# Kernel optimization log

Hardware: AMD Instinct MI355X
Metric: run time of the kernel (lower is better)

## Reference

```python
import jax, jax.numpy as jnp
import numpy as np

EPS = 1e-12
TEMPERATURE = 0.1
QUEUE_SIZE = 1024
CUTOFF_KM = 25.0
EARTH_R_KM = 6371.0088


def _normalize(x, axis=-1):
    n = jnp.linalg.norm(x, axis=axis, keepdims=True)
    return x / jnp.maximum(n, EPS)


def _haversine_km(a, b):
    # a: (B,1,2), b: (1,S,2) in degrees (lat, lon) -> (B,S) km
    ra, rb = jnp.deg2rad(a), jnp.deg2rad(b)
    dlat = rb[..., 0] - ra[..., 0]
    dlon = rb[..., 1] - ra[..., 1]
    h = jnp.sin(dlat / 2) ** 2 + jnp.cos(ra[..., 0]) * jnp.cos(rb[..., 0]) * jnp.sin(dlon / 2) ** 2
    return 2.0 * EARTH_R_KM * jnp.arcsin(jnp.sqrt(jnp.clip(h, 0.0, 1.0)))


def setup_inputs() -> dict:
    key = jax.random.key(0)
    k1, k2, k3, k4, k5 = jax.random.split(key, 5)
    A, B, F, S = 3, 256, 512, 100000
    V = jax.random.normal(k1, (A, B, F), dtype=jnp.float32)
    L = jax.random.normal(k2, (B, F), dtype=jnp.float32)
    # gps as (lat, lon) degrees
    gps = jax.random.uniform(k3, (B, 2), dtype=jnp.float32) * jnp.array([120.0, 360.0]) - jnp.array([60.0, 180.0])
    support_feats = jax.random.normal(k4, (S, F), dtype=jnp.float32)
    support_gps = jax.random.uniform(k5, (S, 2), dtype=jnp.float32) * jnp.array([120.0, 360.0]) - jnp.array([60.0, 180.0])
    return {"V": V, "L": L, "gps": gps, "support_feats": support_feats, "support_gps": support_gps}


def reference(V, L, gps, support_feats, support_gps):
    T, Q = TEMPERATURE, QUEUE_SIZE
    L_norm = _normalize(L, axis=1)                      # (B,F)
    org = _normalize(V[0] * L_norm, axis=1)             # (B,F)
    aug = _normalize(V[1:] * L_norm, axis=2)            # (A-1,B,F)

    # nearest_neighbours (no_grad): per-batch NN in support set by dot-product sim
    sims = jnp.einsum('sf,bf->sb', support_feats, org)  # (S,B)
    nn_idx = jnp.argmax(sims, axis=0)                   # (B,)
    nn = _normalize(support_feats[nn_idx], axis=1)      # (B,F)
    nn = jax.lax.stop_gradient(nn)

    pos = jnp.exp(jnp.einsum('abf,bf->ab', aug, nn) / T)  # (A-1,B)
    batch_den = jnp.sum(pos, axis=0)                       # (B,)

    # nn_negative_queue (no_grad): first Q support rows farther than 25 km, zeros if fewer
    dist = _haversine_km(gps[:, None, :], support_gps[None, :, :])  # (B,S)
    far = dist > CUTOFF_KM                                          # (B,S)
    order = jnp.argsort(jnp.logical_not(far), axis=1)[:, :Q]        # stable: far rows first, in order
    valid = jnp.take_along_axis(far, order, axis=1)                 # (B,Q)
    negq = jnp.where(valid[..., None], support_feats[order], 0.0)   # (B,Q,F)
    negq = jax.lax.stop_gradient(_normalize(negq, axis=2))          # zero rows stay zero

    queue_den = jnp.sum(jnp.exp(jnp.einsum('bqf,bf->bq', negq, nn) / T), axis=1)  # (B,)

    loss = jnp.mean(-batch_den / (batch_den + queue_den))
    return loss
```

## Files before the change

### kernel.cpp

```cpp
#include <hip/hip_runtime.h>
#include <hip/hip_bf16.h>
#include <math.h>

#define B_N 256
#define F_N 512
#define S_N 100000
#define Q_N 1024
#define EPSF 1e-12f
#define BM 128
#define NBLK ((S_N + BM - 1) / BM)
#define CAND_MAX 64
#define MARGIN 0.125f

typedef __attribute__((ext_vector_type(8))) short short8v;
typedef __attribute__((ext_vector_type(4))) float f32x4;

__device__ __forceinline__ unsigned short f2bf(float x) {
  unsigned u = __float_as_uint(x);
  u = u + 0x7FFFu + ((u >> 16) & 1u);
  return (unsigned short)(u >> 16);
}

__device__ __forceinline__ float warpReduceSum(float v) {
  #pragma unroll
  for (int o = 32; o > 0; o >>= 1) v += __shfl_down(v, o);
  return v;
}

__device__ __forceinline__ float blockReduceSum256(float v, float* buf) {
  v = warpReduceSum(v);
  int lane = threadIdx.x & 63, w = threadIdx.x >> 6;
  __syncthreads();
  if (lane == 0) buf[w] = v;
  __syncthreads();
  return buf[0] + buf[1] + buf[2] + buf[3];
}

__device__ __forceinline__ void async_copy16(void* lds, const void* g) {
  __builtin_amdgcn_global_load_lds(
      (const __attribute__((address_space(1))) unsigned int*)g,
      (__attribute__((address_space(3))) unsigned int*)lds, 16, 0, 0);
}

__device__ __forceinline__ void cvt8hi(const float4 a, const float4 b,
                                       short8v& hi) {
  union { unsigned u[4]; short8v v; } H;
  union { __hip_bfloat162 b2; unsigned u; } c;
  c.b2 = __float22bfloat162_rn(make_float2(a.x, a.y)); H.u[0] = c.u;
  c.b2 = __float22bfloat162_rn(make_float2(a.z, a.w)); H.u[1] = c.u;
  c.b2 = __float22bfloat162_rn(make_float2(b.x, b.y)); H.u[2] = c.u;
  c.b2 = __float22bfloat162_rn(make_float2(b.z, b.w)); H.u[3] = c.u;
  hi = H.v;
}

__global__ __launch_bounds__(256) void k_prep(const float* __restrict__ V,
    const float* __restrict__ L, unsigned short* __restrict__ orghi,
    float* __restrict__ org, float* __restrict__ aug) {
  __shared__ float buf[4];
  int b = blockIdx.x, t = threadIdx.x;
  const float2 lv = *(const float2*)&L[b * F_N + t * 2];
  float ss = blockReduceSum256(lv.x * lv.x + lv.y * lv.y, buf);
  float invL = 1.0f / fmaxf(sqrtf(ss), EPSF);
  float lnx = lv.x * invL, lny = lv.y * invL;
  #pragma unroll
  for (int a = 0; a < 3; ++a) {
    const float2 vv = *(const float2*)&V[(a * B_N + b) * F_N + t * 2];
    float yx = vv.x * lnx, yy = vv.y * lny;
    float s2 = blockReduceSum256(yx * yx + yy * yy, buf);
    float inv = 1.0f / fmaxf(sqrtf(s2), EPSF);
    if (a == 0) {
      float ox = yx * inv, oy = yy * inv;
      int f = t * 2;
      int kt = f >> 5, kk = f & 31, sub = kk >> 3, pos = kk & 7;
      int off = kt * 8192 + b * 32 + ((sub ^ ((b >> 1) & 3)) << 3) + pos;
      ushort2 hv; hv.x = f2bf(ox); hv.y = f2bf(oy);
      *(ushort2*)&orghi[off] = hv;
      float2 of; of.x = ox; of.y = oy;
      *(float2*)&org[b * F_N + f] = of;
    } else {
      float* dst = &aug[((a - 1) * B_N + b) * F_N + t * 2];
      dst[0] = yx * inv;
      dst[1] = yy * inv;
    }
  }
}

__global__ __launch_bounds__(256, 2) void k_sims(const float* __restrict__ support,
    const unsigned short* __restrict__ orghi, float* __restrict__ blkmax) {
  __shared__ __align__(16) unsigned char smem[32768];

  int t = threadIdx.x;
  int lane = t & 63, w = t >> 6;
  int r15 = lane & 15, ks = lane >> 4;
  int s0 = blockIdx.x * BM;

  f32x4 acc0[16], acc1[16];
  #pragma unroll
  for (int n = 0; n < 16; ++n) {
    acc0[n] = (f32x4){0.f, 0.f, 0.f, 0.f};
    acc1[n] = (f32x4){0.f, 0.f, 0.f, 0.f};
  }

  int row0 = s0 + w * 32 + r15;
  int row1 = row0 + 16;
  if (row0 > S_N - 1) row0 = S_N - 1;
  if (row1 > S_N - 1) row1 = S_N - 1;
  const float* ap0 = support + (size_t)row0 * F_N + ks * 8;
  const float* ap1 = support + (size_t)row1 * F_N + ks * 8;

  const unsigned char* bsrc = (const unsigned char*)orghi + t * 16;

  {
    unsigned char* dst = smem + t * 16;
    #pragma unroll
    for (int p = 0; p < 4; ++p) async_copy16(dst + p * 4096, bsrc + p * 4096);
  }
  __builtin_amdgcn_sched_barrier(0);
  float4 a0a = *(const float4*)(ap0);
  float4 a0b = *(const float4*)(ap0 + 4);
  float4 a1a = *(const float4*)(ap1);
  float4 a1b = *(const float4*)(ap1 + 4);
  __builtin_amdgcn_sched_barrier(0);
  __syncthreads();

  const int rbase = r15 * 64 + ((ks ^ ((r15 >> 1) & 3)) << 4);

  #pragma unroll 1
  for (int kt = 0; kt < 16; ++kt) {
    unsigned char* bbuf = smem + (kt & 1) * 16384;
    short8v fh0, fh1;
    cvt8hi(a0a, a0b, fh0);
    cvt8hi(a1a, a1b, fh1);
    if (kt < 15) {
      const unsigned char* src = bsrc + (kt + 1) * 16384;
      unsigned char* dst = smem + ((kt + 1) & 1) * 16384 + t * 16;
      #pragma unroll
      for (int p = 0; p < 4; ++p) async_copy16(dst + p * 4096, src + p * 4096);
      __builtin_amdgcn_sched_barrier(0);
      a0a = *(const float4*)(ap0 + (kt + 1) * 32);
      a0b = *(const float4*)(ap0 + (kt + 1) * 32 + 4);
      a1a = *(const float4*)(ap1 + (kt + 1) * 32);
      a1b = *(const float4*)(ap1 + (kt + 1) * 32 + 4);
      __builtin_amdgcn_sched_barrier(0);
    }
    const unsigned char* bp = bbuf + rbase;
    __builtin_amdgcn_s_setprio(1);
    #pragma unroll
    for (int n = 0; n < 16; ++n) {
      short8v bh = *(const short8v*)(bp + n * 1024);
      acc0[n] = __builtin_amdgcn_mfma_f32_16x16x32_bf16(fh0, bh, acc0[n], 0, 0, 0);
      acc1[n] = __builtin_amdgcn_mfma_f32_16x16x32_bf16(fh1, bh, acc1[n], 0, 0, 0);
    }
    __builtin_amdgcn_s_setprio(0);
    __builtin_amdgcn_sched_barrier(0);
    if (kt < 15) {
      asm volatile("s_waitcnt vmcnt(4)" ::: "memory");
      __builtin_amdgcn_s_barrier();
    } else {
      __syncthreads();
    }
    __builtin_amdgcn_sched_barrier(0);
  }

  float* wkf = (float*)smem;
  #pragma unroll
  for (int n = 0; n < 16; ++n) {
    float bv = -INFINITY;
    #pragma unroll
    for (int r = 0; r < 4; ++r) {
      bv = fmaxf(bv, acc0[n][r]);
      bv = fmaxf(bv, acc1[n][r]);
    }
    bv = fmaxf(bv, __shfl_xor(bv, 16));
    bv = fmaxf(bv, __shfl_xor(bv, 32));
    if (lane < 16) wkf[w * 256 + n * 16 + lane] = bv;
  }
  __syncthreads();
  {
    float m4 = fmaxf(fmaxf(wkf[t], wkf[256 + t]),
                     fmaxf(wkf[512 + t], wkf[768 + t]));
    blkmax[(size_t)t * NBLK + blockIdx.x] = m4;
  }
}

__global__ __launch_bounds__(256) void k_picknn(const float* __restrict__ support,
    const float* __restrict__ org, const float* __restrict__ blkmax,
    int* __restrict__ nnidx) {
  __shared__ float orgs[F_N];
  __shared__ float redf[4];
  __shared__ int lcand[CAND_MAX];
  __shared__ int lcnt;
  __shared__ double rv[4];
  __shared__ int ri[4];
  int b = blockIdx.x, t = threadIdx.x;
  int lane = t & 63, w = t >> 6;

  orgs[t] = org[b * F_N + t];
  orgs[256 + t] = org[b * F_N + 256 + t];
  if (t == 0) lcnt = 0;

  const float* bm = blkmax + (size_t)b * NBLK;
  float mx = -INFINITY;
  for (int rb = t; rb < NBLK; rb += 256) mx = fmaxf(mx, bm[rb]);
  #pragma unroll
  for (int o = 32; o > 0; o >>= 1) mx = fmaxf(mx, __shfl_xor(mx, o));
  __syncthreads();
  if (lane == 0) redf[w] = mx;
  __syncthreads();
  mx = fmaxf(fmaxf(redf[0], redf[1]), fmaxf(redf[2], redf[3]));
  float thr = mx - MARGIN;

  for (int rb = t; rb < NBLK; rb += 256) {
    if (bm[rb] >= thr) {
      int sl = atomicAdd(&lcnt, 1);
      if (sl < CAND_MAX) lcand[sl] = rb;
    }
  }
  __syncthreads();
  int nc = lcnt < CAND_MAX ? lcnt : CAND_MAX;

  double bv = -1e300;
  int bi = 0x7FFFFFFF;
  for (int task = t; task < nc * BM; task += 256) {
    int c = task >> 7, r = task & (BM - 1);
    int s = lcand[c] * BM + r;
    if (s < S_N) {
      const float* rp = support + (size_t)s * F_N;
      double d0 = 0, d1 = 0, d2 = 0, d3 = 0;
      #pragma unroll 4
      for (int k = 0; k < F_N; k += 4) {
        d0 += (double)rp[k] * (double)orgs[k];
        d1 += (double)rp[k + 1] * (double)orgs[k + 1];
        d2 += (double)rp[k + 2] * (double)orgs[k + 2];
        d3 += (double)rp[k + 3] * (double)orgs[k + 3];
      }
      double dv = (d0 + d1) + (d2 + d3);
      if (dv > bv || (dv == bv && s < bi)) { bv = dv; bi = s; }
    }
  }
  #pragma unroll
  for (int o = 32; o > 0; o >>= 1) {
    double ov = __shfl_xor(bv, o);
    int oi = __shfl_xor(bi, o);
    if (ov > bv || (ov == bv && oi < bi)) { bv = ov; bi = oi; }
  }
  if (lane == 0) { rv[w] = bv; ri[w] = bi; }
  __syncthreads();
  if (t == 0) {
    double fv = rv[0]; int fi = ri[0];
    #pragma unroll
    for (int i = 1; i < 4; ++i)
      if (rv[i] > fv || (rv[i] == fv && ri[i] < fi)) { fv = rv[i]; fi = ri[i]; }
    nnidx[b] = fi;
  }
}

__global__ __launch_bounds__(256) void k_nn(const float* __restrict__ support,
    const int* __restrict__ nnidx, const float* __restrict__ aug,
    float* __restrict__ nn, float* __restrict__ bden) {
  __shared__ float buf[4];
  int b = blockIdx.x, t = threadIdx.x;
  int idx = nnidx[b];
  const float2 rv = *(const float2*)&support[(size_t)idx * F_N + t * 2];
  float ss = blockReduceSum256(rv.x * rv.x + rv.y * rv.y, buf);
  float inv = 1.0f / fmaxf(sqrtf(ss), EPSF);
  float nx = rv.x * inv, ny = rv.y * inv;
  nn[b * F_N + t * 2] = nx;
  nn[b * F_N + t * 2 + 1] = ny;
  const float2 a0 = *(const float2*)&aug[(0 * B_N + b) * F_N + t * 2];
  const float2 a1 = *(const float2*)&aug[(1 * B_N + b) * F_N + t * 2];
  float d0 = blockReduceSum256(a0.x * nx + a0.y * ny, buf);
  float d1 = blockReduceSum256(a1.x * nx + a1.y * ny, buf);
  if (t == 0) bden[b] = expf(d0 * 10.0f) + expf(d1 * 10.0f);
}

__global__ __launch_bounds__(256) void k_qdot(const float* __restrict__ support,
    const float* __restrict__ gps, const float* __restrict__ sgps,
    const float* __restrict__ nn, double* __restrict__ qpart) {
  __shared__ float nns[F_N];
  __shared__ int qi[256];
  __shared__ int wtot[4];
  __shared__ double wacc[4];
  int b = blockIdx.x >> 2, c = blockIdx.x & 3;
  int t = threadIdx.x;
  int lane = t & 63, w = t >> 6;

  *(float2*)&nns[t * 2] = *(const float2*)&nn[b * F_N + t * 2];

  const float DEG2RAD = 0.017453292519943295f;
  float la = gps[b * 2] * DEG2RAD;
  float lo = gps[b * 2 + 1] * DEG2RAD;
  float ca = cosf(la);
  double xd = 25.0 / (2.0 * 6371.0088);
  float hcut = (float)(sin(xd) * sin(xd));

  int cnt = 0;
  int qlo = c * 256;
  for (int base = 0; base < S_N; base += 256) {
    int s = base + t;
    bool far = false;
    if (s < S_N) {
      float lb = sgps[s * 2] * DEG2RAD;
      float ob = sgps[s * 2 + 1] * DEG2RAD;
      float sl = sinf((lb - la) * 0.5f);
      float so = sinf((ob - lo) * 0.5f);
      float h = sl * sl + ca * cosf(lb) * so * so;
      far = h > hcut;
    }
    unsigned long long m = __ballot(far);
    if (lane == 0) wtot[w] = (int)__popcll(m);
    __syncthreads();
    int offs = cnt;
    for (int wi = 0; wi < w; ++wi) offs += wtot[wi];
    if (far) {
      int pos = offs + (int)__popcll(m & ((1ull << lane) - 1ull));
      int rel = pos - qlo;
      if (rel >= 0 && rel < 256) qi[rel] = s;
    }
    cnt += wtot[0] + wtot[1] + wtot[2] + wtot[3];
    __syncthreads();
    if (cnt >= Q_N) break;
  }
  int nvalid = cnt < Q_N ? cnt : Q_N;
  __syncthreads();

  double acc = 0.0;
  for (int j = 0; j < 64; ++j) {
    int q = qlo + w * 64 + j;
    if (q >= nvalid) break;
    int row = qi[w * 64 + j];
    const float4* rp = (const float4*)&support[(size_t)row * F_N + lane * 8];
    float4 r0 = rp[0], r1 = rp[1];
    const float4 n0 = *(const float4*)&nns[lane * 8];
    const float4 n1 = *(const float4*)&nns[lane * 8 + 4];
    float dot = r0.x * n0.x + r0.y * n0.y + r0.z * n0.z + r0.w * n0.w +
                r1.x * n1.x + r1.y * n1.y + r1.z * n1.z + r1.w * n1.w;
    float ssq = r0.x * r0.x + r0.y * r0.y + r0.z * r0.z + r0.w * r0.w +
                r1.x * r1.x + r1.y * r1.y + r1.z * r1.z + r1.w * r1.w;
    #pragma unroll
    for (int o = 32; o > 0; o >>= 1) {
      dot += __shfl_xor(dot, o);
      ssq += __shfl_xor(ssq, o);
    }
    float val = dot / fmaxf(sqrtf(ssq), EPSF);
    acc += (double)expf(val * 10.0f);
  }
  if (lane == 0) wacc[w] = acc;
  __syncthreads();
  if (t == 0) {
    int got = nvalid - qlo;
    if (got < 0) got = 0; if (got > 256) got = 256;
    int inval = 256 - got;
    qpart[blockIdx.x] = wacc[0] + wacc[1] + wacc[2] + wacc[3] + (double)inval;
  }
}

__global__ __launch_bounds__(256) void k_final(const double* __restrict__ qpart,
    const float* __restrict__ bden, float* __restrict__ out) {
  __shared__ double buf[4];
  int t = threadIdx.x;
  double qd = qpart[t * 4] + qpart[t * 4 + 1] + qpart[t * 4 + 2] + qpart[t * 4 + 3];
  double bd = (double)bden[t];
  double v = -bd / (bd + qd);
  #pragma unroll
  for (int o = 32; o > 0; o >>= 1) v += __shfl_down(v, o);
  if ((t & 63) == 0) buf[t >> 6] = v;
  __syncthreads();
  if (t == 0) out[0] = (float)((buf[0] + buf[1] + buf[2] + buf[3]) / 256.0);
}

extern "C" void kernel_launch(void* const* d_in, const int* in_sizes, int n_in,
                              void* d_out, int out_size, void* d_ws, size_t ws_size,
                              hipStream_t stream) {
  const float* V = (const float*)d_in[0];
  const float* L = (const float*)d_in[1];
  const float* gps = (const float*)d_in[2];
  const float* support = (const float*)d_in[3];
  const float* sgps = (const float*)d_in[4];
  float* out = (float*)d_out;

  char* ws = (char*)d_ws;
  int* nnidx = (int*)ws;
  float* bden = (float*)(ws + 2048);
  double* qpart = (double*)(ws + 4096);
  unsigned short* orghi = (unsigned short*)(ws + 12288);
  float* org = (float*)(ws + 12288 + 262144);
  float* aug = (float*)(ws + 12288 + 262144 + 524288);
  float* nn = (float*)(ws + 12288 + 262144 + 524288 + 1048576);
  float* blkmax = (float*)(ws + 12288 + 262144 + 524288 + 1048576 + 524288);

  k_prep<<<256, 256, 0, stream>>>(V, L, orghi, org, aug);
  k_sims<<<NBLK, 256, 0, stream>>>(support, orghi, blkmax);
  k_picknn<<<256, 256, 0, stream>>>(support, org, blkmax, nnidx);
  k_nn<<<256, 256, 0, stream>>>(support, nnidx, aug, nn, bden);
  k_qdot<<<1024, 256, 0, stream>>>(support, gps, sgps, nn, qpart);
  k_final<<<1, 256, 0, stream>>>(qpart, bden, out);
}
```

Baseline: 191.8 us.

## Read org operand directly from global and use wave-per-row candidate rescoring

The sims kernel stops staging the bf16 org matrix through double-buffered LDS with async copies and barriers, and instead loads each MFMA B fragment straight from global/L2. The swizzled layout in prep is replaced by a plain layout to match. The candidate rescoring is reorganised so each wave handles one support row with coalesced float4 loads and a wave-wide double reduction, instead of one thread scanning a whole row. This removes LDS traffic and barrier stalls but relies on L1/L2 to serve the repeated B fragment reads, which may raise memory latency in the MFMA loop.

```diff
diff --git a/kernel.cpp b/kernel.cpp
--- a/kernel.cpp
+++ b/kernel.cpp
@@ -36,12 +36,6 @@
   return buf[0] + buf[1] + buf[2] + buf[3];
 }
 
-__device__ __forceinline__ void async_copy16(void* lds, const void* g) {
-  __builtin_amdgcn_global_load_lds(
-      (const __attribute__((address_space(1))) unsigned int*)g,
-      (__attribute__((address_space(3))) unsigned int*)lds, 16, 0, 0);
-}
-
 __device__ __forceinline__ void cvt8hi(const float4 a, const float4 b,
                                        short8v& hi) {
   union { unsigned u[4]; short8v v; } H;
@@ -72,7 +66,7 @@
       float ox = yx * inv, oy = yy * inv;
       int f = t * 2;
       int kt = f >> 5, kk = f & 31, sub = kk >> 3, pos = kk & 7;
-      int off = kt * 8192 + b * 32 + ((sub ^ ((b >> 1) & 3)) << 3) + pos;
+      int off = kt * 8192 + b * 32 + sub * 8 + pos;
       ushort2 hv; hv.x = f2bf(ox); hv.y = f2bf(oy);
       *(ushort2*)&orghi[off] = hv;
       float2 of; of.x = ox; of.y = oy;
@@ -87,7 +81,7 @@
 
 __global__ __launch_bounds__(256, 2) void k_sims(const float* __restrict__ support,
     const unsigned short* __restrict__ orghi, float* __restrict__ blkmax) {
-  __shared__ __align__(16) unsigned char smem[32768];
+  __shared__ float wkf[1024];
 
   int t = threadIdx.x;
   int lane = t & 63, w = t >> 6;
@@ -108,42 +102,26 @@
   const float* ap0 = support + (size_t)row0 * F_N + ks * 8;
   const float* ap1 = support + (size_t)row1 * F_N + ks * 8;
 
-  const unsigned char* bsrc = (const unsigned char*)orghi + t * 16;
-
-  {
-    unsigned char* dst = smem + t * 16;
-    #pragma unroll
-    for (int p = 0; p < 4; ++p) async_copy16(dst + p * 4096, bsrc + p * 4096);
-  }
-  __builtin_amdgcn_sched_barrier(0);
+  const unsigned char* bbase =
+      (const unsigned char*)orghi + r15 * 64 + ks * 16;
+
   float4 a0a = *(const float4*)(ap0);
   float4 a0b = *(const float4*)(ap0 + 4);
   float4 a1a = *(const float4*)(ap1);
   float4 a1b = *(const float4*)(ap1 + 4);
-  __builtin_amdgcn_sched_barrier(0);
-  __syncthreads();
-
-  const int rbase = r15 * 64 + ((ks ^ ((r15 >> 1) & 3)) << 4);
 
   #pragma unroll 1
   for (int kt = 0; kt < 16; ++kt) {
-    unsigned char* bbuf = smem + (kt & 1) * 16384;
     short8v fh0, fh1;
     cvt8hi(a0a, a0b, fh0);
     cvt8hi(a1a, a1b, fh1);
     if (kt < 15) {
-      const unsigned char* src = bsrc + (kt + 1) * 16384;
-      unsigned char* dst = smem + ((kt + 1) & 1) * 16384 + t * 16;
-      #pragma unroll
-      for (int p = 0; p < 4; ++p) async_copy16(dst + p * 4096, src + p * 4096);
-      __builtin_amdgcn_sched_barrier(0);
       a0a = *(const float4*)(ap0 + (kt + 1) * 32);
       a0b = *(const float4*)(ap0 + (kt + 1) * 32 + 4);
       a1a = *(const float4*)(ap1 + (kt + 1) * 32);
       a1b = *(const float4*)(ap1 + (kt + 1) * 32 + 4);
-      __builtin_amdgcn_sched_barrier(0);
-    }
-    const unsigned char* bp = bbuf + rbase;
+    }
+    const unsigned char* bp = bbase + kt * 16384;
     __builtin_amdgcn_s_setprio(1);
     #pragma unroll
     for (int n = 0; n < 16; ++n) {
@@ -152,17 +130,8 @@
       acc1[n] = __builtin_amdgcn_mfma_f32_16x16x32_bf16(fh1, bh, acc1[n], 0, 0, 0);
     }
     __builtin_amdgcn_s_setprio(0);
-    __builtin_amdgcn_sched_barrier(0);
-    if (kt < 15) {
-      asm volatile("s_waitcnt vmcnt(4)" ::: "memory");
-      __builtin_amdgcn_s_barrier();
-    } else {
-      __syncthreads();
-    }
-    __builtin_amdgcn_sched_barrier(0);
-  }
-
-  float* wkf = (float*)smem;
+  }
+
   #pragma unroll
   for (int n = 0; n < 16; ++n) {
     float bv = -INFINITY;
@@ -221,28 +190,20 @@
 
   double bv = -1e300;
   int bi = 0x7FFFFFFF;
-  for (int task = t; task < nc * BM; task += 256) {
-    int c = task >> 7, r = task & (BM - 1);
-    int s = lcand[c] * BM + r;
-    if (s < S_N) {
-      const float* rp = support + (size_t)s * F_N;
-      double d0 = 0, d1 = 0, d2 = 0, d3 = 0;
-      #pragma unroll 4
-      for (int k = 0; k < F_N; k += 4) {
-        d0 += (double)rp[k] * (double)orgs[k];
-        d1 += (double)rp[k + 1] * (double)orgs[k + 1];
-        d2 += (double)rp[k + 2] * (double)orgs[k + 2];
-        d3 += (double)rp[k + 3] * (double)orgs[k + 3];
-      }
-      double dv = (d0 + d1) + (d2 + d3);
-      if (dv > bv || (dv == bv && s < bi)) { bv = dv; bi = s; }
-    }
-  }
-  #pragma unroll
-  for (int o = 32; o > 0; o >>= 1) {
-    double ov = __shfl_xor(bv, o);
-    int oi = __shfl_xor(bi, o);
-    if (ov > bv || (ov == bv && oi < bi)) { bv = ov; bi = oi; }
+  for (int rr = w; rr < nc * BM; rr += 4) {
+    int s = lcand[rr >> 7] * BM + (rr & (BM - 1));
+    if (s >= S_N) continue;
+    const float4* rp = (const float4*)(support + (size_t)s * F_N) + lane * 2;
+    float4 r0 = rp[0], r1 = rp[1];
+    const float4 n0 = *(const float4*)&orgs[lane * 8];
+    const float4 n1 = *(const float4*)&orgs[lane * 8 + 4];
+    double d = (double)r0.x * (double)n0.x + (double)r0.y * (double)n0.y +
+               (double)r0.z * (double)n0.z + (double)r0.w * (double)n0.w +
+               (double)r1.x * (double)n1.x + (double)r1.y * (double)n1.y +
+               (double)r1.z * (double)n1.z + (double)r1.w * (double)n1.w;
+    #pragma unroll
+    for (int o = 32; o > 0; o >>= 1) d += __shfl_xor(d, o);
+    if (d > bv || (d == bv && s < bi)) { bv = d; bi = s; }
   }
   if (lane == 0) { rv[w] = bv; ri[w] = bi; }
   __syncthreads();
```

New measurement: 348.1 us. 1.81x slower.
